# Kernel optimization log

Hardware: AMD Instinct MI355X
Metric: run time of the kernel (lower is better)

The kernel has to match this reference:

```python
import jax, jax.numpy as jnp
import numpy as np

VOCAB, EMB, ATT = 100000, 128, 128
N_CODES, N_ANC = 100000, 8

def setup_inputs() -> dict:
    key = jax.random.key(0)
    k1, k2, k3, k4, k5 = jax.random.split(key, 5)
    return {
        "W_emb": jax.random.normal(k1, (VOCAB, EMB), dtype=jnp.float32),
        "W_attention": jax.random.normal(k2, (2 * EMB, ATT), dtype=jnp.float32) * 0.05,
        "b_attention": jnp.zeros((ATT,), dtype=jnp.float32),
        "v_attention": jax.random.normal(k3, (ATT,), dtype=jnp.float32) * 0.05,
        "leaves": jax.random.randint(k4, (N_CODES, N_ANC), 0, VOCAB, dtype=jnp.int64),
        "ancestors": jax.random.randint(k5, (N_CODES, N_ANC), 0, VOCAB, dtype=jnp.int64),
    }

def reference(W_emb, W_attention, b_attention, v_attention, leaves, ancestors):
    # gather: [N, A, E] each
    leave_emb = W_emb[leaves]
    anc_emb = W_emb[ancestors]
    attention_input = jnp.concatenate((leave_emb, anc_emb), axis=2)  # [N, A, 2E]
    mlp = jnp.tanh(jnp.einsum('nae,ed->nad', attention_input, W_attention) + b_attention)
    pre_attention = jnp.einsum('nad,d->na', mlp, v_attention)  # [N, A]
    attn = jax.nn.softmax(pre_attention, axis=1)
    # attention-weighted sum over ancestors: [N, E]
    return jnp.einsum('nae,na->ne', anc_emb, attn)
```

## Files before the change

### kernel.cpp

```cpp
#include <hip/hip_runtime.h>
#include <hip/hip_bf16.h>
#include <hip/hip_fp8.h>

#define VOCAB  100000
#define EMB    128
#define NCODES 100000
#define NANC   8

typedef __attribute__((ext_vector_type(8))) short  short8;
typedef __attribute__((ext_vector_type(4))) float  float4v;
typedef __attribute__((ext_vector_type(2))) float  floatx2;

__device__ __forceinline__ ushort f2bf(float x) {
    unsigned u = __float_as_uint(x);
    u += 0x7fffu + ((u >> 16) & 1u);
    return (ushort)(u >> 16);
}
__device__ __forceinline__ float bf2f(ushort h) {
    return __uint_as_float((unsigned)h << 16);
}
__device__ __forceinline__ float tanh_fast(float x) {
    float e = __expf(2.0f * x);
    return 1.0f - __fdividef(2.0f, e + 1.0f);
}
__device__ __forceinline__ unsigned char f2fp8(float x) {
    __hip_fp8_e4m3 t(x);
    return t.__x;
}
__device__ __forceinline__ unsigned pack_fp8x4(float a, float b, float c, float d) {
#if __has_builtin(__builtin_amdgcn_cvt_pk_fp8_f32)
    int w = __builtin_amdgcn_cvt_pk_fp8_f32(a, b, 0, false);
    w = __builtin_amdgcn_cvt_pk_fp8_f32(c, d, w, true);
    return (unsigned)w;
#else
    return (unsigned)f2fp8(a) | ((unsigned)f2fp8(b) << 8)
         | ((unsigned)f2fp8(c) << 16) | ((unsigned)f2fp8(d) << 24);
#endif
}
template <bool HI>
__device__ __forceinline__ floatx2 fp8pair(unsigned v) {
#if __has_builtin(__builtin_amdgcn_cvt_pk_f32_fp8)
    return __builtin_amdgcn_cvt_pk_f32_fp8((int)v, HI);
#else
    __hip_fp8_e4m3 a, b;
    const unsigned s = HI ? 16u : 0u;
    a.__x = (v >> s) & 0xffu;
    b.__x = (v >> (s + 8u)) & 0xffu;
    floatx2 r; r[0] = (float)a; r[1] = (float)b; return r;
#endif
}

__global__ void transpose_watt(const float* __restrict__ W_att,
                               ushort* __restrict__ WT)
{
    const int id = blockIdx.x * 256 + threadIdx.x;
    const int c = id >> 7, e = id & 127;
    const int h = c >> 7, d = c & 127;
    WT[c * 128 + e] = f2bf(W_att[(h * 128 + e) * 128 + d]);
}

__global__ __launch_bounds__(256) void precompute(
    const float*  __restrict__ W_emb,
    const ushort* __restrict__ WT,
    const float*  __restrict__ b_att,
    unsigned char* __restrict__ P1,
    unsigned char* __restrict__ P2,
    ushort*        __restrict__ Ebf)
{
    const int t = threadIdx.x, wave = t >> 6, lane = t & 63;
    const int n15 = lane & 15, quad = lane >> 4;
    const int cw = wave * 64;

    short8 wfrag[4][4];
    #pragma unroll
    for (int ntl = 0; ntl < 4; ++ntl) {
        const int c = cw + ntl * 16 + n15;
        #pragma unroll
        for (int kt = 0; kt < 4; ++kt)
            wfrag[kt][ntl] = *(const short8*)(WT + c * 128 + kt * 32 + quad * 8);
    }

    float4 bb[4];
    #pragma unroll
    for (int ntl = 0; ntl < 4; ++ntl) {
        if (wave < 2) bb[ntl] = *(const float4*)(b_att + cw + ntl * 16 + quad * 4);
        else          bb[ntl] = make_float4(0.f, 0.f, 0.f, 0.f);
    }

    unsigned char* Pt = (wave < 2) ? P1 : P2;
    const int cofs = ((wave < 2) ? cw : cw - 128) + quad * 4;

    for (int rt = blockIdx.x; rt < VOCAB / 16; rt += gridDim.x) {
        const int R = rt * 16;
        float4v acc[4];
        #pragma unroll
        for (int i = 0; i < 4; ++i) acc[i] = (float4v)0.0f;

        #pragma unroll
        for (int kt = 0; kt < 4; ++kt) {
            const float4* src = (const float4*)(W_emb + (size_t)(R + n15) * 128
                                                + kt * 32 + quad * 8);
            const float4 a0 = src[0], a1 = src[1];
            short8 af;
            af[0] = f2bf(a0.x); af[1] = f2bf(a0.y); af[2] = f2bf(a0.z); af[3] = f2bf(a0.w);
            af[4] = f2bf(a1.x); af[5] = f2bf(a1.y); af[6] = f2bf(a1.z); af[7] = f2bf(a1.w);
            if (wave == 0)
                *(short8*)(Ebf + (size_t)(R + n15) * 128 + kt * 32 + quad * 8) = af;
            #pragma unroll
            for (int ntl = 0; ntl < 4; ++ntl)
                acc[ntl] = __builtin_amdgcn_mfma_f32_16x16x32_bf16(
                               wfrag[kt][ntl], af, acc[ntl], 0, 0, 0);
        }

        #pragma unroll
        for (int ntl = 0; ntl < 4; ++ntl) {
            const unsigned pk = pack_fp8x4(acc[ntl][0] + bb[ntl].x,
                                           acc[ntl][1] + bb[ntl].y,
                                           acc[ntl][2] + bb[ntl].z,
                                           acc[ntl][3] + bb[ntl].w);
            *(unsigned*)(Pt + (size_t)(R + n15) * 128 + cofs + ntl * 16) = pk;
        }
    }
}

__global__ __launch_bounds__(256) void attention_main(
    const unsigned char* __restrict__ P1, const unsigned char* __restrict__ P2,
    const ushort* __restrict__ Ebf,
    const float* __restrict__ v_att,
    const int*   __restrict__ leaves, const int* __restrict__ anc,
    float*       __restrict__ out)
{
    const int t = threadIdx.x;
    const int wave = t >> 6, lane = t & 63;
    const int sub = lane >> 4, l16 = lane & 15;
    const int n = blockIdx.x * 16 + wave * 4 + sub;

    const float4 vva = *(const float4*)(v_att + l16 * 8);
    const float4 vvb = *(const float4*)(v_att + l16 * 8 + 4);

    const int jj = l16 & 7;
    const int lidx = (l16 & 8) ? anc[n * 8 + jj] : leaves[n * 8 + jj];

    int lf[NANC], an[NANC];
    #pragma unroll
    for (int a = 0; a < NANC; ++a) {
        lf[a] = __shfl(lidx, (sub << 4) + a);
        an[a] = __shfl(lidx, (sub << 4) + 8 + a);
    }

    uint2 r1[NANC], r2[NANC];
    short8 em[NANC];
    #pragma unroll
    for (int a = 0; a < NANC; ++a)
        r1[a] = *(const uint2*)(P1 + (size_t)lf[a] * 128 + l16 * 8);
    #pragma unroll
    for (int a = 0; a < NANC; ++a)
        r2[a] = *(const uint2*)(P2 + (size_t)an[a] * 128 + l16 * 8);
    #pragma unroll
    for (int a = 0; a < NANC; ++a)
        em[a] = *(const short8*)(Ebf + (size_t)an[a] * 128 + l16 * 8);

    float q[NANC];
    #pragma unroll
    for (int a = 0; a < NANC; ++a) {
        floatx2 pa, pb;
        float qp;
        pa = fp8pair<false>(r1[a].x); pb = fp8pair<false>(r2[a].x);
        qp  = tanh_fast(pa[0] + pb[0]) * vva.x;
        qp  = fmaf(tanh_fast(pa[1] + pb[1]), vva.y, qp);
        pa = fp8pair<true>(r1[a].x);  pb = fp8pair<true>(r2[a].x);
        qp  = fmaf(tanh_fast(pa[0] + pb[0]), vva.z, qp);
        qp  = fmaf(tanh_fast(pa[1] + pb[1]), vva.w, qp);
        pa = fp8pair<false>(r1[a].y); pb = fp8pair<false>(r2[a].y);
        qp  = fmaf(tanh_fast(pa[0] + pb[0]), vvb.x, qp);
        qp  = fmaf(tanh_fast(pa[1] + pb[1]), vvb.y, qp);
        pa = fp8pair<true>(r1[a].y);  pb = fp8pair<true>(r2[a].y);
        qp  = fmaf(tanh_fast(pa[0] + pb[0]), vvb.z, qp);
        qp  = fmaf(tanh_fast(pa[1] + pb[1]), vvb.w, qp);
        q[a] = qp;
    }

    float r4[4];
    #pragma unroll
    for (int i = 0; i < 4; ++i) {
        const float keep = (l16 & 8) ? q[i + 4] : q[i];
        const float send = (l16 & 8) ? q[i]     : q[i + 4];
        r4[i] = keep + __shfl_xor(send, 8);
    }
    float s2[2];
    #pragma unroll
    for (int i = 0; i < 2; ++i) {
        const float keep = (l16 & 4) ? r4[i + 2] : r4[i];
        const float send = (l16 & 4) ? r4[i]     : r4[i + 2];
        s2[i] = keep + __shfl_xor(send, 4);
    }
    {
        const float keep = (l16 & 2) ? s2[1] : s2[0];
        const float send = (l16 & 2) ? s2[0] : s2[1];
        s2[0] = keep + __shfl_xor(send, 2);
    }
    float tq = s2[0] + __shfl_xor(s2[0], 1);

    float m = tq;
    m = fmaxf(m, __shfl_xor(m, 8));
    m = fmaxf(m, __shfl_xor(m, 4));
    m = fmaxf(m, __shfl_xor(m, 2));
    const float e = __expf(tq - m);
    float s = e;
    s += __shfl_xor(s, 8); s += __shfl_xor(s, 4); s += __shfl_xor(s, 2);
    const float wl = e * __fdividef(1.0f, s);

    float wa[NANC];
    {
        const float p  = __shfl_xor(wl, 2);
        const float w0 = (l16 & 2) ? p  : wl;
        const float w1 = (l16 & 2) ? wl : p;
        const float p0 = __shfl_xor(w0, 4), p1 = __shfl_xor(w1, 4);
        const float v00 = (l16 & 4) ? p0 : w0, v01 = (l16 & 4) ? p1 : w1;
        const float v10 = (l16 & 4) ? w0 : p0, v11 = (l16 & 4) ? w1 : p1;
        float g;
        g = __shfl_xor(v00, 8); wa[0] = (l16 & 8) ? g : v00; wa[4] = (l16 & 8) ? v00 : g;
        g = __shfl_xor(v01, 8); wa[1] = (l16 & 8) ? g : v01; wa[5] = (l16 & 8) ? v01 : g;
        g = __shfl_xor(v10, 8); wa[2] = (l16 & 8) ? g : v10; wa[6] = (l16 & 8) ? v10 : g;
        g = __shfl_xor(v11, 8); wa[3] = (l16 & 8) ? g : v11; wa[7] = (l16 & 8) ? v11 : g;
    }

    float o[8] = {0.f, 0.f, 0.f, 0.f, 0.f, 0.f, 0.f, 0.f};
    #pragma unroll
    for (int a = 0; a < NANC; ++a) {
        #pragma unroll
        for (int c = 0; c < 8; ++c)
            o[c] = fmaf(wa[a], bf2f((ushort)em[a][c]), o[c]);
    }
    float4v o1, o2;
    o1[0] = o[0]; o1[1] = o[1]; o1[2] = o[2]; o1[3] = o[3];
    o2[0] = o[4]; o2[1] = o[5]; o2[2] = o[6]; o2[3] = o[7];
    __builtin_nontemporal_store(o1, (float4v*)(out + (size_t)n * 128 + l16 * 8));
    __builtin_nontemporal_store(o2, (float4v*)(out + (size_t)n * 128 + l16 * 8 + 4));
}

extern "C" void kernel_launch(void* const* d_in, const int* in_sizes, int n_in,
                              void* d_out, int out_size, void* d_ws, size_t ws_size,
                              hipStream_t stream) {
    const float* W_emb  = (const float*)d_in[0];
    const float* W_att  = (const float*)d_in[1];
    const float* b_att  = (const float*)d_in[2];
    const float* v_att  = (const float*)d_in[3];
    const int*   leaves = (const int*)d_in[4];
    const int*   anc    = (const int*)d_in[5];
    float*       out    = (float*)d_out;

    unsigned char* P1 = (unsigned char*)d_ws;
    unsigned char* P2 = P1 + (size_t)VOCAB * 128;
    ushort* Ebf = (ushort*)(P2 + (size_t)VOCAB * 128);
    ushort* WT  = Ebf + (size_t)VOCAB * 128;

    transpose_watt<<<128, 256, 0, stream>>>(W_att, WT);
    precompute<<<1250, 256, 0, stream>>>(W_emb, WT, b_att, P1, P2, Ebf);
    attention_main<<<NCODES / 16, 256, 0, stream>>>(P1, P2, Ebf, v_att,
                                                    leaves, anc, out);
}
```

Before: 218.4 us.

## Use packed rational tanh, packed FMA accumulation, and prefetch W_emb rows in precompute

Replaces the exp-based tanh with a clamped Padé rational approximation, evaluated on float pairs, that shares a single reciprocal across four values. Packed two-wide float math is used for the v-weighted reduction and for the final weighted sum of ancestor embeddings. The precompute kernel now prefetches the next W_emb tile into registers before processing the current one. Together these aim to cut transcendental and ALU instruction counts and hide load latency, at the cost of more registers and slightly lower tanh accuracy near the clamp.

```diff
diff --git a/kernel.cpp b/kernel.cpp
--- a/kernel.cpp
+++ b/kernel.cpp
@@ -18,10 +18,6 @@
 }
 __device__ __forceinline__ float bf2f(ushort h) {
     return __uint_as_float((unsigned)h << 16);
-}
-__device__ __forceinline__ float tanh_fast(float x) {
-    float e = __expf(2.0f * x);
-    return 1.0f - __fdividef(2.0f, e + 1.0f);
 }
 __device__ __forceinline__ unsigned char f2fp8(float x) {
     __hip_fp8_e4m3 t(x);
@@ -50,6 +46,27 @@
 #endif
 }
 
+__device__ __forceinline__ void tanh2pk(floatx2 za, floatx2 zb,
+                                        floatx2& ta, floatx2& tb) {
+    floatx2 xa, xb;
+    xa[0] = fminf(fmaxf(za[0], -3.5f), 3.5f);
+    xa[1] = fminf(fmaxf(za[1], -3.5f), 3.5f);
+    xb[0] = fminf(fmaxf(zb[0], -3.5f), 3.5f);
+    xb[1] = fminf(fmaxf(zb[1], -3.5f), 3.5f);
+    const floatx2 ya = xa * xa, yb = xb * xb;
+    floatx2 Na = ya + 105.0f;  Na = ya * Na + 945.0f;
+    floatx2 Nb = yb + 105.0f;  Nb = yb * Nb + 945.0f;
+    floatx2 Da = ya * 15.0f + 420.0f;  Da = ya * Da + 945.0f;
+    floatx2 Db = yb * 15.0f + 420.0f;  Db = yb * Db + 945.0f;
+    const floatx2 Dp = Da * Db;
+    const float r = __builtin_amdgcn_rcpf(Dp[0] * Dp[1]);
+    floatx2 qv;  qv[0] = r * Dp[1];  qv[1] = r * Dp[0];
+    const floatx2 ia = qv * Db;
+    const floatx2 ib = qv * Da;
+    ta = (xa * Na) * ia;
+    tb = (xb * Nb) * ib;
+}
+
 __global__ void transpose_watt(const float* __restrict__ W_att,
                                ushort* __restrict__ WT)
 {
@@ -90,7 +107,30 @@
     unsigned char* Pt = (wave < 2) ? P1 : P2;
     const int cofs = ((wave < 2) ? cw : cw - 128) + quad * 4;
 
-    for (int rt = blockIdx.x; rt < VOCAB / 16; rt += gridDim.x) {
+    const int NT = VOCAB / 16;
+    int rt = blockIdx.x;
+    float4 cur[8];
+    {
+        const float4* src = (const float4*)(W_emb + (size_t)(rt * 16 + n15) * 128);
+        #pragma unroll
+        for (int kt = 0; kt < 4; ++kt) {
+            cur[2 * kt]     = src[kt * 8 + quad * 2];
+            cur[2 * kt + 1] = src[kt * 8 + quad * 2 + 1];
+        }
+    }
+
+    for (; rt < NT; ) {
+        const int nrt = rt + gridDim.x;
+        float4 nxt[8];
+        if (nrt < NT) {
+            const float4* src = (const float4*)(W_emb + (size_t)(nrt * 16 + n15) * 128);
+            #pragma unroll
+            for (int kt = 0; kt < 4; ++kt) {
+                nxt[2 * kt]     = src[kt * 8 + quad * 2];
+                nxt[2 * kt + 1] = src[kt * 8 + quad * 2 + 1];
+            }
+        }
+
         const int R = rt * 16;
         float4v acc[4];
         #pragma unroll
@@ -98,9 +138,7 @@
 
         #pragma unroll
         for (int kt = 0; kt < 4; ++kt) {
-            const float4* src = (const float4*)(W_emb + (size_t)(R + n15) * 128
-                                                + kt * 32 + quad * 8);
-            const float4 a0 = src[0], a1 = src[1];
+            const float4 a0 = cur[2 * kt], a1 = cur[2 * kt + 1];
             short8 af;
             af[0] = f2bf(a0.x); af[1] = f2bf(a0.y); af[2] = f2bf(a0.z); af[3] = f2bf(a0.w);
             af[4] = f2bf(a1.x); af[5] = f2bf(a1.y); af[6] = f2bf(a1.z); af[7] = f2bf(a1.w);
@@ -120,6 +158,10 @@
                                            acc[ntl][3] + bb[ntl].w);
             *(unsigned*)(Pt + (size_t)(R + n15) * 128 + cofs + ntl * 16) = pk;
         }
+
+        rt = nrt;
+        #pragma unroll
+        for (int i = 0; i < 8; ++i) cur[i] = nxt[i];
     }
 }
 
@@ -135,8 +177,10 @@
     const int sub = lane >> 4, l16 = lane & 15;
     const int n = blockIdx.x * 16 + wave * 4 + sub;
 
-    const float4 vva = *(const float4*)(v_att + l16 * 8);
-    const float4 vvb = *(const float4*)(v_att + l16 * 8 + 4);
+    floatx2 vv[4];
+    #pragma unroll
+    for (int p = 0; p < 4; ++p)
+        vv[p] = *(const floatx2*)(v_att + l16 * 8 + 2 * p);
 
     const int jj = l16 & 7;
     const int lidx = (l16 & 8) ? anc[n * 8 + jj] : leaves[n * 8 + jj];
@@ -163,21 +207,18 @@
     float q[NANC];
     #pragma unroll
     for (int a = 0; a < NANC; ++a) {
-        floatx2 pa, pb;
-        float qp;
-        pa = fp8pair<false>(r1[a].x); pb = fp8pair<false>(r2[a].x);
-        qp  = tanh_fast(pa[0] + pb[0]) * vva.x;
-        qp  = fmaf(tanh_fast(pa[1] + pb[1]), vva.y, qp);
-        pa = fp8pair<true>(r1[a].x);  pb = fp8pair<true>(r2[a].x);
-        qp  = fmaf(tanh_fast(pa[0] + pb[0]), vva.z, qp);
-        qp  = fmaf(tanh_fast(pa[1] + pb[1]), vva.w, qp);
-        pa = fp8pair<false>(r1[a].y); pb = fp8pair<false>(r2[a].y);
-        qp  = fmaf(tanh_fast(pa[0] + pb[0]), vvb.x, qp);
-        qp  = fmaf(tanh_fast(pa[1] + pb[1]), vvb.y, qp);
-        pa = fp8pair<true>(r1[a].y);  pb = fp8pair<true>(r2[a].y);
-        qp  = fmaf(tanh_fast(pa[0] + pb[0]), vvb.z, qp);
-        qp  = fmaf(tanh_fast(pa[1] + pb[1]), vvb.w, qp);
-        q[a] = qp;
+        const floatx2 z0 = fp8pair<false>(r1[a].x) + fp8pair<false>(r2[a].x);
+        const floatx2 z1 = fp8pair<true >(r1[a].x) + fp8pair<true >(r2[a].x);
+        const floatx2 z2 = fp8pair<false>(r1[a].y) + fp8pair<false>(r2[a].y);
+        const floatx2 z3 = fp8pair<true >(r1[a].y) + fp8pair<true >(r2[a].y);
+        floatx2 t0, t1, t2, t3;
+        tanh2pk(z0, z1, t0, t1);
+        tanh2pk(z2, z3, t2, t3);
+        floatx2 qa = t0 * vv[0];
+        qa = t1 * vv[1] + qa;
+        qa = t2 * vv[2] + qa;
+        qa = t3 * vv[3] + qa;
+        q[a] = qa[0] + qa[1];
     }
 
     float r4[4];
@@ -225,16 +266,21 @@
         g = __shfl_xor(v11, 8); wa[3] = (l16 & 8) ? g : v11; wa[7] = (l16 & 8) ? v11 : g;
     }
 
-    float o[8] = {0.f, 0.f, 0.f, 0.f, 0.f, 0.f, 0.f, 0.f};
+    floatx2 o[4] = {(floatx2)0.f, (floatx2)0.f, (floatx2)0.f, (floatx2)0.f};
     #pragma unroll
     for (int a = 0; a < NANC; ++a) {
-        #pragma unroll
-        for (int c = 0; c < 8; ++c)
-            o[c] = fmaf(wa[a], bf2f((ushort)em[a][c]), o[c]);
+        floatx2 wv; wv[0] = wa[a]; wv[1] = wa[a];
+        #pragma unroll
+        for (int p = 0; p < 4; ++p) {
+            floatx2 ev;
+            ev[0] = bf2f((ushort)em[a][2 * p]);
+            ev[1] = bf2f((ushort)em[a][2 * p + 1]);
+            o[p] = ev * wv + o[p];
+        }
     }
     float4v o1, o2;
-    o1[0] = o[0]; o1[1] = o[1]; o1[2] = o[2]; o1[3] = o[3];
-    o2[0] = o[4]; o2[1] = o[5]; o2[2] = o[6]; o2[3] = o[7];
+    o1[0] = o[0][0]; o1[1] = o[0][1]; o1[2] = o[1][0]; o1[3] = o[1][1];
+    o2[0] = o[2][0]; o2[1] = o[2][1]; o2[2] = o[3][0]; o2[3] = o[3][1];
     __builtin_nontemporal_store(o1, (float4v*)(out + (size_t)n * 128 + l16 * 8));
     __builtin_nontemporal_store(o2, (float4v*)(out + (size_t)n * 128 + l16 * 8 + 4));
 }
```

Result: faster. 199.6 us (-8.6%).
